# Performance work log

Measured on AMD Instinct MI355X. Metric: run time of the kernel, lower is better.

Reference implementation:

```python
import jax, jax.numpy as jnp
import numpy as np

MAX_NORM = 10.0
NUM_LAYERS = 3
MARGIN = 0.1
VAE_BETA = 0.1
EPS = 1e-7
N_NODES = 100000


def logmap0(x):
    # Lorentz (k=1) log map at origin: first coord -> 0, spatial scaled
    x0 = x[..., :1]
    alpha = jnp.maximum(x0, 1.0 + EPS)
    coef = jnp.arccosh(alpha) / jnp.sqrt(jnp.maximum(alpha * alpha - 1.0, EPS))
    return jnp.concatenate([jnp.zeros_like(x0), coef * x[..., 1:]], axis=-1)


def expmap0(u, project=False):
    # Lorentz (k=1) exp map at origin; first coord of u is ignored (tangent at o)
    sp = u[..., 1:]
    n = jnp.maximum(jnp.linalg.norm(sp, axis=-1, keepdims=True), EPS)
    x_sp = jnp.sinh(n) / n * sp
    if project:
        sn = jnp.linalg.norm(x_sp, axis=-1, keepdims=True)
        x_sp = x_sp * jnp.minimum(1.0, MAX_NORM / jnp.maximum(sn, EPS))
        x0 = jnp.sqrt(1.0 + jnp.sum(x_sp * x_sp, axis=-1, keepdims=True))
    else:
        x0 = jnp.cosh(n)
    return jnp.concatenate([x0, x_sp], axis=-1)


def sqdist(x, y):
    inner = -x[..., 0] * y[..., 0] + jnp.sum(x[..., 1:] * y[..., 1:], axis=-1)
    d = jnp.arccosh(jnp.maximum(-inner, 1.0 + EPS))
    return d * d


def moe(x, W, b, gW, gb):
    gates = jax.nn.softmax(x @ gW + gb, axis=-1)              # [N,E]
    expert = jnp.einsum('nd,edo->neo', x, W) + b               # [N,E,D]
    return jnp.einsum('neo,ne->no', expert, gates)             # [N,D]


def spmm(rows, cols, vals, h):
    return jax.ops.segment_sum(vals[:, None] * h[cols], rows, num_segments=N_NODES)


def setup_inputs() -> dict:
    key = jax.random.key(0)
    ks = jax.random.split(key, 24)
    D, E, NNZ, T = 64, 8, 3200000, 262144
    Nu, Ni = 60000, 40000
    s = 0.05
    emb_user = expmap0(jax.random.normal(ks[0], (Nu, D)) * 0.1, project=True)
    emb_item = expmap0(jax.random.normal(ks[1], (Ni, D)) * 0.1, project=True)
    return {
        'emb_user': emb_user,
        'emb_item': emb_item,
        'adj_rows': jax.random.randint(ks[2], (NNZ,), 0, N_NODES, dtype=jnp.int32),
        'adj_cols': jax.random.randint(ks[3], (NNZ,), 0, N_NODES, dtype=jnp.int32),
        'adj_vals': jax.random.uniform(ks[4], (NNZ,)) * 0.05,
        'triples': jax.random.randint(ks[5], (T, 3), 0, N_NODES, dtype=jnp.int32),
        'eps': jax.random.normal(ks[6], (N_NODES, D)),
        'tW': jax.random.normal(ks[7], (E, D, D)) * s,
        'tb': jax.random.normal(ks[8], (E, D)) * s,
        'tgW': jax.random.normal(ks[9], (D, E)) * s,
        'tgb': jax.random.normal(ks[10], (E,)) * s,
        'muW': jax.random.normal(ks[11], (D, D)) * s,
        'mub': jax.random.normal(ks[12], (D,)) * s,
        'lvW': jax.random.normal(ks[13], (D, D)) * s,
        'lvb': jax.random.normal(ks[14], (D,)) * s,
        'f1W': jax.random.normal(ks[15], (D, 2 * D)) * s,
        'f1b': jax.random.normal(ks[16], (2 * D,)) * s,
        'f2W': jax.random.normal(ks[17], (2 * D, D)) * s,
        'f2b': jax.random.normal(ks[18], (D,)) * s,
        'dW': jax.random.normal(ks[19], (E, D, D)) * s,
        'db': jax.random.normal(ks[20], (E, D)) * s,
        'dgW': jax.random.normal(ks[21], (D, E)) * s,
        'dgb': jax.random.normal(ks[22], (E,)) * s,
    }


def reference(emb_user, emb_item, adj_rows, adj_cols, adj_vals, triples, eps,
              tW, tb, tgW, tgb, muW, mub, lvW, lvb,
              f1W, f1b, f2W, f2b, dW, db, dgW, dgb):
    # encode: log map frozen hyperbolic embeddings, MoE transform
    t = jnp.concatenate([logmap0(emb_user), logmap0(emb_item)], axis=0)   # [N,D]
    m = moe(t, tW, tb, tgW, tgb)                                          # [N,D]
    # VAE
    mu = m @ muW + mub
    logvar = m @ lvW + lvb
    std = jnp.exp(0.5 * logvar)
    z = expmap0(mu + eps * std, project=True)
    # hyperbolic decoder
    h = logmap0(z)
    h = jax.nn.relu(h @ f1W + f1b)
    h = h @ f2W + f2b
    h = moe(h, dW, db, dgW, dgb)
    recon = expmap0(h, project=True)
    recon_loss = jnp.mean(sqdist(recon, expmap0(m)))
    kl_loss = -0.5 * jnp.mean(1.0 + logvar - mu * mu - jnp.exp(logvar))
    # margin loss: num_layers of sparse propagation, sum of layer outputs
    res = m
    out_sum = jnp.zeros_like(m)
    for _ in range(NUM_LAYERS):
        res = spmm(adj_rows, adj_cols, adj_vals, res)
        out_sum = out_sum + res
    out = expmap0(out_sum, project=True)
    a, p, n = out[triples[:, 0]], out[triples[:, 1]], out[triples[:, 2]]
    margin_loss = jnp.sum(jax.nn.relu(sqdist(a, p) - sqdist(a, n) + MARGIN))
    return margin_loss + VAE_BETA * (recon_loss + kl_loss)
```

## Files before the change

### kernel.cpp

```cpp
#include <hip/hip_runtime.h>
#include <math.h>

#define EPSF 1e-7f
#define MAXNRM 10.0f
#define NB 782
#define RPB 128
#define EPT 16

using bf16x8 = __attribute__((ext_vector_type(8))) short;
using f32x4  = __attribute__((ext_vector_type(4))) float;

__device__ __forceinline__ float wsum(float v) {
    #pragma unroll
    for (int off = 32; off > 0; off >>= 1) v += __shfl_xor(v, off, 64);
    return v;
}

__device__ __forceinline__ unsigned short f2bf(float x) {
    unsigned u = __float_as_uint(x);
    unsigned r = (u + 0x7FFFu + ((u >> 16) & 1u)) >> 16;
    return (unsigned short)r;
}
__device__ __forceinline__ float bflo(unsigned u) { return __uint_as_float(u << 16); }
__device__ __forceinline__ float bfhi(unsigned u) { return __uint_as_float(u & 0xFFFF0000u); }

__global__ __launch_bounds__(256) void k_logmap(const float* __restrict__ eu, const float* __restrict__ ei,
                                                int Nu, int Ntot, float* __restrict__ out) {
    const int lane = threadIdx.x & 63;
    const int g = lane >> 4, q = lane & 15;
    const int n = blockIdx.x * 16 + (threadIdx.x >> 6) * 4 + g;
    if (n >= Ntot) return;
    const float* src = (n < Nu) ? (eu + (size_t)n * 64) : (ei + (size_t)(n - Nu) * 64);
    const float x0 = src[0];
    const float alpha = fmaxf(x0, 1.0f + EPSF);
    const float coef = acoshf(alpha) / sqrtf(fmaxf(alpha * alpha - 1.0f, EPSF));
    const float4 v = *(const float4*)(src + q * 4);
    float4 o;
    o.x = (q == 0) ? 0.0f : coef * v.x;
    o.y = coef * v.y; o.z = coef * v.z; o.w = coef * v.w;
    *(float4*)(out + ((size_t)n << 6) + q * 4) = o;
}

__global__ __launch_bounds__(256) void k_prep(const float* __restrict__ W, const float* __restrict__ Bb,
                                              unsigned short* __restrict__ Wt, unsigned short* __restrict__ Bt) {
    const int i = blockIdx.x * 256 + threadIdx.x;
    if (i < 4096) {
        const int e = i >> 9, o = (i >> 3) & 63, db = i & 7;
        unsigned short v[8];
        #pragma unroll
        for (int j = 0; j < 8; ++j)
            v[j] = f2bf(W[((size_t)e << 12) + (size_t)(db * 8 + j) * 64 + o]);
        uint4 p;
        p.x = (unsigned)v[0] | ((unsigned)v[1] << 16);
        p.y = (unsigned)v[2] | ((unsigned)v[3] << 16);
        p.z = (unsigned)v[4] | ((unsigned)v[5] << 16);
        p.w = (unsigned)v[6] | ((unsigned)v[7] << 16);
        *(uint4*)(Wt + (((size_t)(e * 64 + o)) << 6) + db * 8) = p;
    } else if (i < 4096 + 512) {
        const int j = i - 4096, o = j >> 3, e = j & 7;
        Bt[o * 8 + e] = f2bf(Bb[e * 64 + o]);
    }
}

__global__ __launch_bounds__(256) void k_prepw(const float* __restrict__ src,
                                               unsigned short* __restrict__ dst, int K, int O) {
    const int i = blockIdx.x * 256 + threadIdx.x;
    if (i >= K * O) return;
    const int o = i / K, k = i - o * K;
    dst[i] = f2bf(src[k * O + o]);
}

__global__ __launch_bounds__(256) void k_moe_mfma(
    const float* __restrict__ X, float* __restrict__ Y,
    const unsigned short* __restrict__ Wt, const unsigned short* __restrict__ Bt,
    const float* __restrict__ GW, const float* __restrict__ GB,
    unsigned short* __restrict__ Bhout, int Ntot)
{
    __shared__ float sX[64][68];
    __shared__ float sG[64][8];
    __shared__ float sGW[512];
    const int tid = threadIdx.x;
    const int n0 = blockIdx.x * 64;

    for (int i = tid; i < 64 * 16; i += 256) {
        const int rr = i >> 4, cc = i & 15;
        float4 v = make_float4(0.f, 0.f, 0.f, 0.f);
        if (n0 + rr < Ntot) v = *(const float4*)(X + (size_t)(n0 + rr) * 64 + cc * 4);
        *(float4*)&sX[rr][cc * 4] = v;
    }
    for (int i = tid; i < 512; i += 256) sGW[i] = GW[i];
    __syncthreads();

    {
        const int n = tid >> 2, e0 = (tid & 3) * 2;
        float lg0 = GB[e0], lg1 = GB[e0 + 1];
        #pragma unroll 8
        for (int d = 0; d < 64; ++d) {
            const float xv = sX[n][d];
            lg0 += xv * sGW[d * 8 + e0];
            lg1 += xv * sGW[d * 8 + e0 + 1];
        }
        sG[n][e0] = lg0; sG[n][e0 + 1] = lg1;
    }
    __syncthreads();
    if (tid < 64) {
        float ex[8], mx = -1e30f, s = 0.f;
        #pragma unroll
        for (int e = 0; e < 8; ++e) mx = fmaxf(mx, sG[tid][e]);
        #pragma unroll
        for (int e = 0; e < 8; ++e) { ex[e] = expf(sG[tid][e] - mx); s += ex[e]; }
        const float inv = 1.0f / s;
        #pragma unroll
        for (int e = 0; e < 8; ++e) sG[tid][e] = ex[e] * inv;
    }
    __syncthreads();

    const int w = tid >> 6, l = tid & 63;
    const int m = l & 15, kq = l >> 4;
    const int col = w * 16 + m;

    f32x4 zero = {0.f, 0.f, 0.f, 0.f};
    f32x4 acc[4];
    #pragma unroll
    for (int rt = 0; rt < 4; ++rt) acc[rt] = zero;

    bf16x8 bcur = *(const bf16x8*)(Wt + (((size_t)col) << 6) + kq * 8);

    #pragma unroll
    for (int kk = 0; kk < 16; ++kk) {
        const int e = kk >> 1;
        const int d0 = (kk & 1) * 32 + kq * 8;
        bf16x8 bnext = bcur;
        if (kk < 15) {
            const int e2 = (kk + 1) >> 1;
            const int d02 = ((kk + 1) & 1) * 32 + kq * 8;
            bnext = *(const bf16x8*)(Wt + (((size_t)(e2 * 64 + col)) << 6) + d02);
        }
        #pragma unroll
        for (int rt = 0; rt < 4; ++rt) {
            const int row = rt * 16 + m;
            const float gme = sG[row][e];
            const float4 xa = *(const float4*)&sX[row][d0];
            const float4 xb = *(const float4*)&sX[row][d0 + 4];
            union { bf16x8 v; unsigned short u[8]; } af;
            af.u[0] = f2bf(gme * xa.x); af.u[1] = f2bf(gme * xa.y);
            af.u[2] = f2bf(gme * xa.z); af.u[3] = f2bf(gme * xa.w);
            af.u[4] = f2bf(gme * xb.x); af.u[5] = f2bf(gme * xb.y);
            af.u[6] = f2bf(gme * xb.z); af.u[7] = f2bf(gme * xb.w);
            acc[rt] = __builtin_amdgcn_mfma_f32_16x16x32_bf16(af.v, bcur, acc[rt], 0, 0, 0);
        }
        bcur = bnext;
    }
    {
        bf16x8 z8 = {0, 0, 0, 0, 0, 0, 0, 0};
        bf16x8 bb = z8;
        if (kq == 0) bb = *(const bf16x8*)(Bt + (col << 3));
        #pragma unroll
        for (int rt = 0; rt < 4; ++rt) {
            union { bf16x8 v; unsigned short u[8]; } af;
            #pragma unroll
            for (int j = 0; j < 8; ++j)
                af.u[j] = (kq == 0) ? f2bf(sG[rt * 16 + m][j]) : (unsigned short)0;
            acc[rt] = __builtin_amdgcn_mfma_f32_16x16x32_bf16(af.v, bb, acc[rt], 0, 0, 0);
        }
    }

    #pragma unroll
    for (int rt = 0; rt < 4; ++rt) {
        #pragma unroll
        for (int r = 0; r < 4; ++r) {
            const int row = rt * 16 + kq * 4 + r;
            if (n0 + row < Ntot) {
                Y[(size_t)(n0 + row) * 64 + col] = acc[rt][r];
                if (Bhout)
                    Bhout[(((size_t)(n0 + row)) << 6) + col] = f2bf(acc[rt][r]);
            }
        }
    }
}

__global__ __launch_bounds__(256) void k_vae_mfma(
    const float* __restrict__ M, float* __restrict__ Hout,
    const float* __restrict__ EPSN, const unsigned short* __restrict__ WtV,
    const float* __restrict__ mub, const float* __restrict__ lvb,
    float* __restrict__ klslot, int Ntot)
{
    __shared__ float sX[64][68];
    __shared__ float sC[64];
    const int tid = threadIdx.x;
    const int n0 = blockIdx.x * 64;

    for (int i = tid; i < 64 * 16; i += 256) {
        const int rr = i >> 4, cc = i & 15;
        float4 v = make_float4(0.f, 0.f, 0.f, 0.f);
        if (n0 + rr < Ntot) v = *(const float4*)(M + (size_t)(n0 + rr) * 64 + cc * 4);
        *(float4*)&sX[rr][cc * 4] = v;
    }
    __syncthreads();

    const int w = tid >> 6, l = tid & 63;
    const int m = l & 15, kq = l >> 4;
    const int rowm = w * 16 + m;

    f32x4 zero = {0.f, 0.f, 0.f, 0.f};
    f32x4 acc[8];
    #pragma unroll
    for (int t = 0; t < 8; ++t) acc[t] = zero;

    #pragma unroll
    for (int ks = 0; ks < 2; ++ks) {
        const int k0 = ks * 32 + kq * 8;
        const float4 xa = *(const float4*)&sX[rowm][k0];
        const float4 xb = *(const float4*)&sX[rowm][k0 + 4];
        union { bf16x8 v; unsigned short u[8]; } af;
        af.u[0] = f2bf(xa.x); af.u[1] = f2bf(xa.y); af.u[2] = f2bf(xa.z); af.u[3] = f2bf(xa.w);
        af.u[4] = f2bf(xb.x); af.u[5] = f2bf(xb.y); af.u[6] = f2bf(xb.z); af.u[7] = f2bf(xb.w);
        #pragma unroll
        for (int t = 0; t < 8; ++t) {
            const bf16x8 bf = *(const bf16x8*)(WtV + (((size_t)(t * 16 + m)) << 6) + k0);
            acc[t] = __builtin_amdgcn_mfma_f32_16x16x32_bf16(af.v, bf, acc[t], 0, 0, 0);
        }
    }

    float klp = 0.f;
    float uv[4][4];
    #pragma unroll
    for (int t = 0; t < 4; ++t) {
        const int col = t * 16 + m;
        const float mb = mub[col], lb = lvb[col];
        #pragma unroll
        for (int r = 0; r < 4; ++r) {
            const int row = w * 16 + kq * 4 + r;
            const float mu = acc[t][r] + mb;
            const float lv = acc[t + 4][r] + lb;
            const float elv = expf(lv);
            float ep = 0.f;
            if (n0 + row < Ntot) {
                klp += 1.0f + lv - mu * mu - elv;
                ep = EPSN[(size_t)(n0 + row) * 64 + col];
            }
            uv[t][r] = mu + ep * expf(0.5f * lv);
        }
    }
    klp = wsum(klp);
    if (l == 0) atomicAdd(&klslot[(blockIdx.x * 4 + w) & 255], klp);

    #pragma unroll
    for (int t = 0; t < 4; ++t)
        #pragma unroll
        for (int r = 0; r < 4; ++r)
            sX[w * 16 + kq * 4 + r][t * 16 + m] = uv[t][r];
    __syncthreads();

    {
        const int r2 = tid >> 2, j = tid & 3;
        float ss = 0.f;
        #pragma unroll
        for (int jj = 0; jj < 4; ++jj) {
            float4 a = *(const float4*)&sX[r2][j * 16 + jj * 4];
            if (j == 0 && jj == 0) a.x = 0.f;
            ss += a.x * a.x + a.y * a.y + a.z * a.z + a.w * a.w;
        }
        ss += __shfl_xor(ss, 1, 64);
        ss += __shfl_xor(ss, 2, 64);
        if (j == 0) {
            const float nr = fmaxf(sqrtf(ss), EPSF);
            const float r = sinhf(nr) / nr;
            const float sn = r * sqrtf(ss);
            const float scale = fminf(1.0f, MAXNRM / fmaxf(sn, EPSF));
            const float mult = r * scale;
            const float s2 = mult * mult * ss;
            const float z0 = sqrtf(1.0f + s2);
            const float alpha = fmaxf(z0, 1.0f + EPSF);
            const float coef = acoshf(alpha) / sqrtf(fmaxf(alpha * alpha - 1.0f, EPSF));
            sC[r2] = coef * mult;
        }
    }
    __syncthreads();

    for (int i = tid; i < 64 * 16; i += 256) {
        const int rr = i >> 4, cc = i & 15;
        if (n0 + rr >= Ntot) continue;
        const float4 v = *(const float4*)&sX[rr][cc * 4];
        const float sc = sC[rr];
        float4 o;
        o.x = (cc == 0) ? 0.f : sc * v.x;
        o.y = sc * v.y; o.z = sc * v.z; o.w = sc * v.w;
        *(float4*)(Hout + (size_t)(n0 + rr) * 64 + cc * 4) = o;
    }
}

__global__ __launch_bounds__(256) void k_ffn_mfma(
    float* __restrict__ Hio,
    const unsigned short* __restrict__ Wt1f, const float* __restrict__ f1b,
    const unsigned short* __restrict__ Wt2f, const float* __restrict__ f2b, int Ntot)
{
    __shared__ float sH[64][68];
    __shared__ unsigned short sH1[64][136];
    const int tid = threadIdx.x;
    const int n0 = blockIdx.x * 64;

    for (int i = tid; i < 64 * 16; i += 256) {
        const int rr = i >> 4, cc = i & 15;
        float4 v = make_float4(0.f, 0.f, 0.f, 0.f);
        if (n0 + rr < Ntot) v = *(const float4*)(Hio + (size_t)(n0 + rr) * 64 + cc * 4);
        *(float4*)&sH[rr][cc * 4] = v;
    }
    __syncthreads();

    const int w = tid >> 6, l = tid & 63;
    const int m = l & 15, kq = l >> 4;
    const int rowm = w * 16 + m;

    f32x4 zero = {0.f, 0.f, 0.f, 0.f};
    f32x4 acc1[8];
    #pragma unroll
    for (int t = 0; t < 8; ++t) acc1[t] = zero;

    #pragma unroll
    for (int ks = 0; ks < 2; ++ks) {
        const int k0 = ks * 32 + kq * 8;
        const float4 xa = *(const float4*)&sH[rowm][k0];
        const float4 xb = *(const float4*)&sH[rowm][k0 + 4];
        union { bf16x8 v; unsigned short u[8]; } af;
        af.u[0] = f2bf(xa.x); af.u[1] = f2bf(xa.y); af.u[2] = f2bf(xa.z); af.u[3] = f2bf(xa.w);
        af.u[4] = f2bf(xb.x); af.u[5] = f2bf(xb.y); af.u[6] = f2bf(xb.z); af.u[7] = f2bf(xb.w);
        #pragma unroll
        for (int t = 0; t < 8; ++t) {
            const bf16x8 bf = *(const bf16x8*)(Wt1f + (((size_t)(t * 16 + m)) << 6) + k0);
            acc1[t] = __builtin_amdgcn_mfma_f32_16x16x32_bf16(af.v, bf, acc1[t], 0, 0, 0);
        }
    }
    #pragma unroll
    for (int t = 0; t < 8; ++t) {
        const float bb = f1b[t * 16 + m];
        #pragma unroll
        for (int r = 0; r < 4; ++r)
            sH1[w * 16 + kq * 4 + r][t * 16 + m] = f2bf(fmaxf(acc1[t][r] + bb, 0.f));
    }
    __syncthreads();

    f32x4 acc2[4];
    #pragma unroll
    for (int t = 0; t < 4; ++t) acc2[t] = zero;
    #pragma unroll
    for (int ks = 0; ks < 4; ++ks) {
        const int k0 = ks * 32 + kq * 8;
        const bf16x8 af = *(const bf16x8*)&sH1[rowm][k0];
        #pragma unroll
        for (int t = 0; t < 4; ++t) {
            const bf16x8 bf = *(const bf16x8*)(Wt2f + (((size_t)(t * 16 + m)) << 7) + k0);
            acc2[t] = __builtin_amdgcn_mfma_f32_16x16x32_bf16(af, bf, acc2[t], 0, 0, 0);
        }
    }
    #pragma unroll
    for (int t = 0; t < 4; ++t) {
        const float bb = f2b[t * 16 + m];
        #pragma unroll
        for (int r = 0; r < 4; ++r) {
            const int row = w * 16 + kq * 4 + r;
            if (n0 + row < Ntot)
                Hio[(size_t)(n0 + row) * 64 + t * 16 + m] = acc2[t][r] + bb;
        }
    }
}

__global__ __launch_bounds__(256) void k_recon(
    const float* __restrict__ HM, const float* __restrict__ M,
    int Ntot, float* __restrict__ slot)
{
    const int lane = threadIdx.x & 63;
    const int g = lane >> 4, q = lane & 15;
    const int n = blockIdx.x * 16 + (threadIdx.x >> 6) * 4 + g;

    float ssh = 0.f, ssm = 0.f, dot = 0.f;
    if (n < Ntot) {
        const float4 h = *(const float4*)(HM + ((size_t)n << 6) + q * 4);
        const float4 m = *(const float4*)(M  + ((size_t)n << 6) + q * 4);
        const float hx = (q == 0) ? 0.f : h.x;
        const float mx = (q == 0) ? 0.f : m.x;
        ssh = hx * hx + h.y * h.y + h.z * h.z + h.w * h.w;
        ssm = mx * mx + m.y * m.y + m.z * m.z + m.w * m.w;
        dot = hx * mx + h.y * m.y + h.z * m.z + h.w * m.w;
    }
    #pragma unroll
    for (int off = 1; off < 16; off <<= 1) {
        ssh += __shfl_xor(ssh, off, 64);
        ssm += __shfl_xor(ssm, off, 64);
        dot += __shfl_xor(dot, off, 64);
    }

    float part = 0.f;
    if (q == 0 && n < Ntot) {
        const float nm = fmaxf(sqrtf(ssm), EPSF);
        const float em0 = coshf(nm);
        const float rm = sinhf(nm) / nm;

        const float nh = fmaxf(sqrtf(ssh), EPSF);
        const float rh = sinhf(nh) / nh;
        const float sn = rh * sqrtf(ssh);
        const float scale = fminf(1.0f, MAXNRM / fmaxf(sn, EPSF));
        const float mult = rh * scale;
        const float rec0 = sqrtf(1.0f + mult * mult * ssh);

        const float inner = mult * rm * dot - rec0 * em0;
        const float dd = acoshf(fmaxf(-inner, 1.0f + EPSF));
        part = dd * dd;
    }
    part = wsum(part);
    __shared__ float sb[4];
    if (lane == 0) sb[threadIdx.x >> 6] = part;
    __syncthreads();
    if (threadIdx.x == 0)
        atomicAdd(&slot[blockIdx.x & 255], sb[0] + sb[1] + sb[2] + sb[3]);
}

__global__ __launch_bounds__(256) void k_bhist(const int* __restrict__ rows, int nnz,
                                               int* __restrict__ bhist) {
    __shared__ int h[NB];
    for (int j = threadIdx.x; j < NB; j += 256) h[j] = 0;
    __syncthreads();
    for (int i = blockIdx.x * 256 + threadIdx.x; i < nnz; i += gridDim.x * 256)
        atomicAdd(&h[rows[i] >> 7], 1);
    __syncthreads();
    for (int j = threadIdx.x; j < NB; j += 256)
        if (h[j]) atomicAdd(&bhist[j], h[j]);
}

__global__ __launch_bounds__(1024) void k_bscan(const int* __restrict__ bhist,
                                                int* __restrict__ bstart, int* __restrict__ gcur) {
    __shared__ int s[1024];
    const int tid = threadIdx.x;
    int v = (tid < NB) ? bhist[tid] : 0;
    s[tid] = v;
    __syncthreads();
    for (int off = 1; off < 1024; off <<= 1) {
        int t = (tid >= off) ? s[tid - off] : 0;
        __syncthreads();
        s[tid] += t;
        __syncthreads();
    }
    if (tid < NB) {
        bstart[tid + 1] = s[tid];
        gcur[tid] = s[tid] - v;
        if (tid == 0) bstart[0] = 0;
    }
}

__global__ __launch_bounds__(256) void k_bscatter(
    const int* __restrict__ rows, const int* __restrict__ cols,
    const float* __restrict__ vals, int nnz,
    int* __restrict__ gcur, int2* __restrict__ tmp)
{
    __shared__ int lh[NB];
    __shared__ int lb[NB];
    const int tid = threadIdx.x;
    for (int j = tid; j < NB; j += 256) lh[j] = 0;
    __syncthreads();

    const int base = blockIdx.x * (256 * EPT);
    int r[EPT], c[EPT], lp[EPT];
    float v[EPT];
    #pragma unroll
    for (int j = 0; j < EPT; ++j) {
        const int i = base + j * 256 + tid;
        if (i < nnz) {
            r[j] = rows[i]; c[j] = cols[i]; v[j] = vals[i];
            lp[j] = atomicAdd(&lh[r[j] >> 7], 1);
        }
    }
    __syncthreads();
    for (int j = tid; j < NB; j += 256)
        if (lh[j]) lb[j] = atomicAdd(&gcur[j], lh[j]);
    __syncthreads();
    #pragma unroll
    for (int j = 0; j < EPT; ++j) {
        const int i = base + j * 256 + tid;
        if (i < nnz) {
            int2 e;
            e.x = ((r[j] & 127) << 17) | c[j];
            e.y = __float_as_int(v[j]);
            tmp[lb[r[j] >> 7] + lp[j]] = e;
        }
    }
}

__global__ __launch_bounds__(256) void k_sort(
    const int2* __restrict__ tmp, const int* __restrict__ bstart,
    int2* __restrict__ sedge, int* __restrict__ Fout, int Ntot, int nnz)
{
    __shared__ int cnt[RPB];
    __shared__ int excl[RPB];
    const int b = blockIdx.x;
    const int tid = threadIdx.x;
    if (tid < RPB) cnt[tid] = 0;
    __syncthreads();
    const int s = bstart[b], t = bstart[b + 1];

    for (int i = s + tid; i < t; i += 256)
        atomicAdd(&cnt[((unsigned)tmp[i].x) >> 17], 1);
    __syncthreads();

    if (tid < 64) {
        const int a0 = cnt[2 * tid], a1 = cnt[2 * tid + 1];
        const int pairsum = a0 + a1;
        int run = pairsum;
        #pragma unroll
        for (int off = 1; off < 64; off <<= 1) {
            const int vv = __shfl_up(run, off, 64);
            if (tid >= off) run += vv;
        }
        const int ep = run - pairsum;
        excl[2 * tid] = ep;
        excl[2 * tid + 1] = ep + a0;
    }
    __syncthreads();

    const int r0 = b << 7;
    if (tid < RPB) {
        const int r = r0 + tid;
        if (r < Ntot) Fout[r] = s + excl[tid];
        cnt[tid] = excl[tid];
    }
    if (b == NB - 1 && tid == 0) Fout[Ntot] = nnz;
    __syncthreads();

    for (int i = s + tid; i < t; i += 256) {
        const int2 e = tmp[i];
        const int rib = ((unsigned)e.x) >> 17;
        const int lpos = atomicAdd(&cnt[rib], 1);
        int2 o; o.x = e.x & 0x1FFFF; o.y = e.y;
        sedge[s + lpos] = o;
    }
}

__global__ __launch_bounds__(256) void k_spmm(
    const unsigned short* __restrict__ in, unsigned short* __restrict__ outb,
    const int* __restrict__ F, const int2* __restrict__ sedge, int Ntot, int nnz)
{
    const int r = blockIdx.x * 4 + (threadIdx.x >> 6);
    if (r >= Ntot) return;
    const int lane = threadIdx.x & 63;
    const int g = lane >> 3, q = lane & 7;
    const int e0 = F[r], e1 = F[r + 1];
    const int nnzm1 = nnz - 1;

    float acc0[8], acc1[8];
    #pragma unroll
    for (int j = 0; j < 8; ++j) { acc0[j] = 0.f; acc1[j] = 0.f; }

    int2 edA, edB;
    uint4 hbA, hbB;
    {
        const int ea = e0 + g, eb = e0 + 8 + g;
        edA = sedge[min(ea, nnzm1)]; if (ea >= e1) edA.y = 0;
        edB = sedge[min(eb, nnzm1)]; if (eb >= e1) edB.y = 0;
        hbA = *(const uint4*)(in + (((size_t)edA.x) << 6) + q * 8);
        hbB = *(const uint4*)(in + (((size_t)edB.x) << 6) + q * 8);
    }

    for (int base = e0; base < e1; base += 16) {
        const int na = base + 16 + g, nb = base + 24 + g;
        int2 edA2 = sedge[min(na, nnzm1)]; if (na >= e1) edA2.y = 0;
        int2 edB2 = sedge[min(nb, nnzm1)]; if (nb >= e1) edB2.y = 0;
        const uint4 hbA2 = *(const uint4*)(in + (((size_t)edA2.x) << 6) + q * 8);
        const uint4 hbB2 = *(const uint4*)(in + (((size_t)edB2.x) << 6) + q * 8);

        {
            const float v = __int_as_float(edA.y);
            acc0[0] += v * bflo(hbA.x);
            acc0[1] += v * bfhi(hbA.x);
            acc0[2] += v * bflo(hbA.y);
            acc0[3] += v * bfhi(hbA.y);
            acc0[4] += v * bflo(hbA.z);
            acc0[5] += v * bfhi(hbA.z);
            acc0[6] += v * bflo(hbA.w);
            acc0[7] += v * bfhi(hbA.w);
        }
        {
            const float v = __int_as_float(edB.y);
            acc1[0] += v * bflo(hbB.x);
            acc1[1] += v * bfhi(hbB.x);
            acc1[2] += v * bflo(hbB.y);
            acc1[3] += v * bfhi(hbB.y);
            acc1[4] += v * bflo(hbB.z);
            acc1[5] += v * bfhi(hbB.z);
            acc1[6] += v * bflo(hbB.w);
            acc1[7] += v * bfhi(hbB.w);
        }
        edA = edA2; edB = edB2; hbA = hbA2; hbB = hbB2;
    }
    float a0[8];
    #pragma unroll
    for (int j = 0; j < 8; ++j) a0[j] = acc0[j] + acc1[j];

    #pragma unroll
    for (int off = 8; off < 64; off <<= 1)
        #pragma unroll
        for (int j = 0; j < 8; ++j) a0[j] += __shfl_xor(a0[j], off, 64);

    if (g == 0) {
        const size_t ob = (((size_t)r) << 6) + q * 8;
        uint4 p;
        p.x = (unsigned)f2bf(a0[0]) | ((unsigned)f2bf(a0[1]) << 16);
        p.y = (unsigned)f2bf(a0[2]) | ((unsigned)f2bf(a0[3]) << 16);
        p.z = (unsigned)f2bf(a0[4]) | ((unsigned)f2bf(a0[5]) << 16);
        p.w = (unsigned)f2bf(a0[6]) | ((unsigned)f2bf(a0[7]) << 16);
        *(uint4*)(outb + ob) = p;
    }
}

__global__ __launch_bounds__(256) void k_osum(
    const unsigned short* __restrict__ r1, const unsigned short* __restrict__ r2,
    const unsigned short* __restrict__ r3, unsigned short* __restrict__ outb, int Ntot)
{
    const int lane = threadIdx.x & 63;
    const int g = lane >> 4, q = lane & 15;
    const int n = blockIdx.x * 16 + (threadIdx.x >> 6) * 4 + g;
    if (n >= Ntot) return;
    const size_t ob = ((size_t)n << 6) + q * 4;
    const uint2 a = *(const uint2*)(r1 + ob);
    const uint2 b = *(const uint2*)(r2 + ob);
    const uint2 c = *(const uint2*)(r3 + ob);
    float s0 = bflo(a.x) + bflo(b.x) + bflo(c.x);
    float s1 = bfhi(a.x) + bfhi(b.x) + bfhi(c.x);
    float s2 = bflo(a.y) + bflo(b.y) + bflo(c.y);
    float s3 = bfhi(a.y) + bfhi(b.y) + bfhi(c.y);
    const float v0 = (q == 0) ? 0.f : s0;
    float ss = v0 * v0 + s1 * s1 + s2 * s2 + s3 * s3;
    #pragma unroll
    for (int off = 1; off < 16; off <<= 1) ss += __shfl_xor(ss, off, 64);
    const float nr = fmaxf(sqrtf(ss), EPSF);
    const float r = sinhf(nr) / nr;
    const float sn = r * sqrtf(ss);
    const float scale = fminf(1.0f, MAXNRM / fmaxf(sn, EPSF));
    const float mult = r * scale;
    const float o0 = (q == 0) ? sqrtf(1.0f + mult * mult * ss) : mult * s0;
    uint2 p;
    p.x = (unsigned)f2bf(o0) | ((unsigned)f2bf(mult * s1) << 16);
    p.y = (unsigned)f2bf(mult * s2) | ((unsigned)f2bf(mult * s3) << 16);
    *(uint2*)(outb + ob) = p;
}

__global__ __launch_bounds__(256) void k_triples(
    const unsigned short* __restrict__ Ob, const int* __restrict__ tri,
    int T, float* __restrict__ slot)
{
    const int lane = threadIdx.x & 63;
    const int g = lane >> 4, q = lane & 15;
    const int wid = blockIdx.x * 4 + (threadIdx.x >> 6);
    const int stride = gridDim.x * 4 * 4;

    float racc = 0.f;
    int t = wid * 4 + g;

    uint2 ca, cp, cn;
    if (t < T) {
        const int a = tri[3 * t], p = tri[3 * t + 1], nn = tri[3 * t + 2];
        ca = *(const uint2*)(Ob + (((size_t)a) << 6) + q * 4);
        cp = *(const uint2*)(Ob + (((size_t)p) << 6) + q * 4);
        cn = *(const uint2*)(Ob + (((size_t)nn) << 6) + q * 4);
    }

    for (; t < T; ) {
        const int tn = t + stride;
        const int tc = min(tn, T - 1);
        const int a2 = tri[3 * tc], p2 = tri[3 * tc + 1], n2 = tri[3 * tc + 2];
        const uint2 na_ = *(const uint2*)(Ob + (((size_t)a2) << 6) + q * 4);
        const uint2 np_ = *(const uint2*)(Ob + (((size_t)p2) << 6) + q * 4);
        const uint2 nn_ = *(const uint2*)(Ob + (((size_t)n2) << 6) + q * 4);

        {
            const float a0 = bflo(ca.x), a1 = bfhi(ca.x), a2f = bflo(ca.y), a3 = bfhi(ca.y);
            const float p0 = bflo(cp.x), p1 = bfhi(cp.x), p2f = bflo(cp.y), p3 = bfhi(cp.y);
            const float n0 = bflo(cn.x), n1 = bfhi(cn.x), n2f = bflo(cn.y), n3 = bfhi(cn.y);
            const float s0 = (q == 0) ? -1.f : 1.f;
            float i1 = s0 * a0 * p0 + a1 * p1 + a2f * p2f + a3 * p3;
            float i2 = s0 * a0 * n0 + a1 * n1 + a2f * n2f + a3 * n3;
            #pragma unroll
            for (int off = 1; off < 16; off <<= 1) {
                i1 += __shfl_xor(i1, off, 64);
                i2 += __shfl_xor(i2, off, 64);
            }
            if (q == 0) {
                const float d1 = acoshf(fmaxf(-i1, 1.0f + EPSF));
                const float d2 = acoshf(fmaxf(-i2, 1.0f + EPSF));
                const float l = d1 * d1 - d2 * d2 + 0.1f;
                if (l > 0.f) racc += l;
            }
        }
        ca = na_; cp = np_; cn = nn_;
        t = tn;
    }

    racc = wsum(racc);
    __shared__ float sb[4];
    if (lane == 0) sb[threadIdx.x >> 6] = racc;
    __syncthreads();
// ... 14 lines not shown
        const float R = sr[0] + sr[1] + sr[2] + sr[3];
        const float K = sk[0] + sk[1] + sk[2] + sk[3];
        const float recon = R / (float)Ntot;
        const float kl = -0.5f * K / ((float)Ntot * 64.0f);
        out[0] = M + 0.1f * (recon + kl);
    }
}

extern "C" void kernel_launch(void* const* d_in, const int* in_sizes, int n_in,
                              void* d_out, int out_size, void* d_ws, size_t ws_size,
                              hipStream_t stream)
{
    const float* emb_user = (const float*)d_in[0];
    const float* emb_item = (const float*)d_in[1];
    const int*   adj_rows = (const int*)d_in[2];
    const int*   adj_cols = (const int*)d_in[3];
    const float* adj_vals = (const float*)d_in[4];
    const int*   triples  = (const int*)d_in[5];
    const float* epsin    = (const float*)d_in[6];
    const float* tW  = (const float*)d_in[7];
    const float* tb  = (const float*)d_in[8];
    const float* tgW = (const float*)d_in[9];
    const float* tgb = (const float*)d_in[10];
    const float* muW = (const float*)d_in[11];
    const float* mub = (const float*)d_in[12];
    const float* lvW = (const float*)d_in[13];
    const float* lvb = (const float*)d_in[14];
    const float* f1W = (const float*)d_in[15];
    const float* f1b = (const float*)d_in[16];
    const float* f2W = (const float*)d_in[17];
    const float* f2b = (const float*)d_in[18];
    const float* dW  = (const float*)d_in[19];
    const float* db  = (const float*)d_in[20];
    const float* dgW = (const float*)d_in[21];
    const float* dgb = (const float*)d_in[22];

    const int Nu = in_sizes[0] / 64, Ni = in_sizes[1] / 64;
    const int N = Nu + Ni;
    const int NNZ = in_sizes[4];
    const int T = in_sizes[5] / 3;

    float* ws = (float*)d_ws;
    size_t off = 0;
    float* slots = ws + off; off += 1024;
    float* A  = ws + off; off += (size_t)N * 64;
    float* B  = ws + off; off += (size_t)N * 64;
    float* C  = ws + off; off += (size_t)N * 64;
    float* D  = ws + off; off += (size_t)N * 64;
    float* E  = ws + off; off += (size_t)N * 64;
    int*   F  = (int*)(ws + off); off += (size_t)N + 64;
    int*   bstart = (int*)(ws + off); off += 1024;
    int*   bhist  = (int*)(ws + off); off += 1024;
    int*   gcur   = (int*)(ws + off); off += 1024;
    unsigned short* Wt1 = (unsigned short*)(ws + off); off += 16384;
    unsigned short* Bt1 = (unsigned short*)(ws + off); off += 256;
    unsigned short* Wt2 = (unsigned short*)(ws + off); off += 16384;
    unsigned short* Bt2 = (unsigned short*)(ws + off); off += 256;
    unsigned short* WtV  = (unsigned short*)(ws + off); off += 4096;
    unsigned short* Wt1f = (unsigned short*)(ws + off); off += 4096;
    unsigned short* Wt2f = (unsigned short*)(ws + off); off += 4096;

    int2* tmp   = (int2*)A;
    int2* sedge = (int2*)D;
    unsigned short* Bh  = (unsigned short*)E;
    unsigned short* Hb1 = (unsigned short*)E + (size_t)N * 64;
    unsigned short* Hb2 = (unsigned short*)C;
    unsigned short* Hb3 = (unsigned short*)A;
    unsigned short* Ob  = (unsigned short*)B;

    hipMemsetAsync(slots, 0, 1024 * sizeof(float), stream);
    hipMemsetAsync(bhist, 0, 1024 * sizeof(int), stream);

    const int nb16 = (N + 15) / 16;
    const int nb64 = (N + 63) / 64;

    k_prep<<<18, 256, 0, stream>>>(tW, tb, Wt1, Bt1);
    k_prep<<<18, 256, 0, stream>>>(dW, db, Wt2, Bt2);
    k_prepw<<<16, 256, 0, stream>>>(muW, WtV, 64, 64);
    k_prepw<<<16, 256, 0, stream>>>(lvW, WtV + 4096, 64, 64);
    k_prepw<<<32, 256, 0, stream>>>(f1W, Wt1f, 64, 128);
    k_prepw<<<32, 256, 0, stream>>>(f2W, Wt2f, 128, 64);

    k_logmap<<<nb16, 256, 0, stream>>>(emb_user, emb_item, Nu, N, A);
    k_moe_mfma<<<nb64, 256, 0, stream>>>(A, B, Wt1, Bt1, tgW, tgb, Bh, N);
    k_vae_mfma<<<nb64, 256, 0, stream>>>(B, A, epsin, WtV, mub, lvb, slots + 512, N);
    k_ffn_mfma<<<nb64, 256, 0, stream>>>(A, Wt1f, f1b, Wt2f, f2b, N);
    k_moe_mfma<<<nb64, 256, 0, stream>>>(A, C, Wt2, Bt2, dgW, dgb, nullptr, N);
    k_recon<<<nb16, 256, 0, stream>>>(C, B, N, slots + 256);

    k_bhist<<<512, 256, 0, stream>>>(adj_rows, NNZ, bhist);
    k_bscan<<<1, 1024, 0, stream>>>(bhist, bstart, gcur);
    const int ns1 = (NNZ + 256 * EPT - 1) / (256 * EPT);
    k_bscatter<<<ns1, 256, 0, stream>>>(adj_rows, adj_cols, adj_vals, NNZ, gcur, tmp);
    k_sort<<<NB, 256, 0, stream>>>(tmp, bstart, sedge, F, N, NNZ);

    k_spmm<<<(N + 3) / 4, 256, 0, stream>>>(Bh,  Hb1, F, sedge, N, NNZ);
    k_spmm<<<(N + 3) / 4, 256, 0, stream>>>(Hb1, Hb2, F, sedge, N, NNZ);
    k_spmm<<<(N + 3) / 4, 256, 0, stream>>>(Hb2, Hb3, F, sedge, N, NNZ);

    k_osum<<<nb16, 256, 0, stream>>>(Hb1, Hb2, Hb3, Ob, N);

    k_triples<<<2048, 256, 0, stream>>>(Ob, triples, T, slots);
    k_final<<<1, 256, 0, stream>>>(slots, (float*)d_out, N);
}
```

Measured before the change: 513.2 us.

## Fuse independent dense and sparse-sort kernels into combined launches

Merges the six weight-prep kernels into one launch. It also pairs independent stages into 'fat' kernels that dispatch on block index: logmap with the row histogram, encoder MoE with the bucket scatter, and VAE with the per-bucket sort. The goal is to cut launch count and let the memory-bound CSR build overlap with the MFMA-heavy dense stages. The tmp buffer moves from A to C so it does not collide with buffers live in the merged stages. The merged kernels share one shared-memory size, which may lower occupancy for the lighter branches.

```diff
diff --git a/kernel.cpp b/kernel.cpp
--- a/kernel.cpp
+++ b/kernel.cpp
@@ -9,6 +9,7 @@
 
 using bf16x8 = __attribute__((ext_vector_type(8))) short;
 using f32x4  = __attribute__((ext_vector_type(4))) float;
+typedef unsigned short u16;
 
 __device__ __forceinline__ float wsum(float v) {
     #pragma unroll
@@ -16,19 +17,21 @@
     return v;
 }
 
-__device__ __forceinline__ unsigned short f2bf(float x) {
+__device__ __forceinline__ u16 f2bf(float x) {
     unsigned u = __float_as_uint(x);
     unsigned r = (u + 0x7FFFu + ((u >> 16) & 1u)) >> 16;
-    return (unsigned short)r;
+    return (u16)r;
 }
 __device__ __forceinline__ float bflo(unsigned u) { return __uint_as_float(u << 16); }
 __device__ __forceinline__ float bfhi(unsigned u) { return __uint_as_float(u & 0xFFFF0000u); }
 
-__global__ __launch_bounds__(256) void k_logmap(const float* __restrict__ eu, const float* __restrict__ ei,
-                                                int Nu, int Ntot, float* __restrict__ out) {
+
+__device__ __forceinline__ void body_logmap(int bid, const float* __restrict__ eu,
+                                            const float* __restrict__ ei, int Nu, int Ntot,
+                                            float* __restrict__ out) {
     const int lane = threadIdx.x & 63;
     const int g = lane >> 4, q = lane & 15;
-    const int n = blockIdx.x * 16 + (threadIdx.x >> 6) * 4 + g;
+    const int n = bid * 16 + (threadIdx.x >> 6) * 4 + g;
     if (n >= Ntot) return;
     const float* src = (n < Nu) ? (eu + (size_t)n * 64) : (ei + (size_t)(n - Nu) * 64);
     const float x0 = src[0];
@@ -41,46 +44,28 @@
     *(float4*)(out + ((size_t)n << 6) + q * 4) = o;
 }
 
-__global__ __launch_bounds__(256) void k_prep(const float* __restrict__ W, const float* __restrict__ Bb,
-                                              unsigned short* __restrict__ Wt, unsigned short* __restrict__ Bt) {
-    const int i = blockIdx.x * 256 + threadIdx.x;
-    if (i < 4096) {
-        const int e = i >> 9, o = (i >> 3) & 63, db = i & 7;
-        unsigned short v[8];
-        #pragma unroll
-        for (int j = 0; j < 8; ++j)
-            v[j] = f2bf(W[((size_t)e << 12) + (size_t)(db * 8 + j) * 64 + o]);
-        uint4 p;
-        p.x = (unsigned)v[0] | ((unsigned)v[1] << 16);
-        p.y = (unsigned)v[2] | ((unsigned)v[3] << 16);
-        p.z = (unsigned)v[4] | ((unsigned)v[5] << 16);
-        p.w = (unsigned)v[6] | ((unsigned)v[7] << 16);
-        *(uint4*)(Wt + (((size_t)(e * 64 + o)) << 6) + db * 8) = p;
-    } else if (i < 4096 + 512) {
-        const int j = i - 4096, o = j >> 3, e = j & 7;
-        Bt[o * 8 + e] = f2bf(Bb[e * 64 + o]);
-    }
-}
-
-__global__ __launch_bounds__(256) void k_prepw(const float* __restrict__ src,
-                                               unsigned short* __restrict__ dst, int K, int O) {
-    const int i = blockIdx.x * 256 + threadIdx.x;
-    if (i >= K * O) return;
-    const int o = i / K, k = i - o * K;
-    dst[i] = f2bf(src[k * O + o]);
-}
-
-__global__ __launch_bounds__(256) void k_moe_mfma(
+__device__ __forceinline__ void body_bhist(int bid, int nblk, const int* __restrict__ rows,
+                                           int nnz, int* __restrict__ bhist, int* h) {
+    for (int j = threadIdx.x; j < NB; j += 256) h[j] = 0;
+    __syncthreads();
+    for (int i = bid * 256 + threadIdx.x; i < nnz; i += nblk * 256)
+        atomicAdd(&h[rows[i] >> 7], 1);
+    __syncthreads();
+    for (int j = threadIdx.x; j < NB; j += 256)
+        if (h[j]) atomicAdd(&bhist[j], h[j]);
+}
+
+__device__ __forceinline__ void body_moe(int bid, char* smem,
     const float* __restrict__ X, float* __restrict__ Y,
-    const unsigned short* __restrict__ Wt, const unsigned short* __restrict__ Bt,
+    const u16* __restrict__ Wt, const u16* __restrict__ Bt,
     const float* __restrict__ GW, const float* __restrict__ GB,
-    unsigned short* __restrict__ Bhout, int Ntot)
-{
-    __shared__ float sX[64][68];
-    __shared__ float sG[64][8];
-    __shared__ float sGW[512];
+    u16* __restrict__ Bhout, int Ntot)
+{
+    float (*sX)[68] = (float(*)[68])smem;
+    float (*sG)[8]  = (float(*)[8])(smem + 17408);
+    float* sGW      = (float*)(smem + 17408 + 2048);
     const int tid = threadIdx.x;
-    const int n0 = blockIdx.x * 64;
+    const int n0 = bid * 64;
 
     for (int i = tid; i < 64 * 16; i += 256) {
         const int rr = i >> 4, cc = i & 15;
@@ -142,7 +127,7 @@
             const float gme = sG[row][e];
             const float4 xa = *(const float4*)&sX[row][d0];
             const float4 xb = *(const float4*)&sX[row][d0 + 4];
-            union { bf16x8 v; unsigned short u[8]; } af;
+            union { bf16x8 v; u16 u[8]; } af;
             af.u[0] = f2bf(gme * xa.x); af.u[1] = f2bf(gme * xa.y);
             af.u[2] = f2bf(gme * xa.z); af.u[3] = f2bf(gme * xa.w);
             af.u[4] = f2bf(gme * xb.x); af.u[5] = f2bf(gme * xb.y);
@@ -157,10 +142,10 @@
         if (kq == 0) bb = *(const bf16x8*)(Bt + (col << 3));
         #pragma unroll
         for (int rt = 0; rt < 4; ++rt) {
-            union { bf16x8 v; unsigned short u[8]; } af;
+            union { bf16x8 v; u16 u[8]; } af;
             #pragma unroll
             for (int j = 0; j < 8; ++j)
-                af.u[j] = (kq == 0) ? f2bf(sG[rt * 16 + m][j]) : (unsigned short)0;
+                af.u[j] = (kq == 0) ? f2bf(sG[rt * 16 + m][j]) : (u16)0;
             acc[rt] = __builtin_amdgcn_mfma_f32_16x16x32_bf16(af.v, bb, acc[rt], 0, 0, 0);
         }
     }
@@ -179,16 +164,54 @@
     }
 }
 
-__global__ __launch_bounds__(256) void k_vae_mfma(
+__device__ __forceinline__ void body_bscatter(int bid, char* smem,
+    const int* __restrict__ rows, const int* __restrict__ cols,
+    const float* __restrict__ vals, int nnz,
+    int* __restrict__ gcur, int2* __restrict__ tmp)
+{
+    int* lh = (int*)smem;
+    int* lb = (int*)(smem + 3128);
+    const int tid = threadIdx.x;
+    for (int j = tid; j < NB; j += 256) lh[j] = 0;
+    __syncthreads();
+
+    const int base = bid * (256 * EPT);
+    int r[EPT], c[EPT], lp[EPT];
+    float v[EPT];
+    #pragma unroll
+    for (int j = 0; j < EPT; ++j) {
+        const int i = base + j * 256 + tid;
+        if (i < nnz) {
+            r[j] = rows[i]; c[j] = cols[i]; v[j] = vals[i];
+            lp[j] = atomicAdd(&lh[r[j] >> 7], 1);
+        }
+    }
+    __syncthreads();
+    for (int j = tid; j < NB; j += 256)
+        if (lh[j]) lb[j] = atomicAdd(&gcur[j], lh[j]);
+    __syncthreads();
+    #pragma unroll
+    for (int j = 0; j < EPT; ++j) {
+        const int i = base + j * 256 + tid;
+        if (i < nnz) {
+            int2 e;
+            e.x = ((r[j] & 127) << 17) | c[j];
+            e.y = __float_as_int(v[j]);
+            tmp[lb[r[j] >> 7] + lp[j]] = e;
+        }
+    }
+}
+
+__device__ __forceinline__ void body_vae(int bid, char* smem,
     const float* __restrict__ M, float* __restrict__ Hout,
-    const float* __restrict__ EPSN, const unsigned short* __restrict__ WtV,
+    const float* __restrict__ EPSN, const u16* __restrict__ WtV,
     const float* __restrict__ mub, const float* __restrict__ lvb,
     float* __restrict__ klslot, int Ntot)
 {
-    __shared__ float sX[64][68];
-    __shared__ float sC[64];
+    float (*sX)[68] = (float(*)[68])smem;
+    float* sC       = (float*)(smem + 17408);
     const int tid = threadIdx.x;
-    const int n0 = blockIdx.x * 64;
+    const int n0 = bid * 64;
 
     for (int i = tid; i < 64 * 16; i += 256) {
         const int rr = i >> 4, cc = i & 15;
@@ -212,7 +235,7 @@
         const int k0 = ks * 32 + kq * 8;
         const float4 xa = *(const float4*)&sX[rowm][k0];
         const float4 xb = *(const float4*)&sX[rowm][k0 + 4];
-        union { bf16x8 v; unsigned short u[8]; } af;
+        union { bf16x8 v; u16 u[8]; } af;
         af.u[0] = f2bf(xa.x); af.u[1] = f2bf(xa.y); af.u[2] = f2bf(xa.z); af.u[3] = f2bf(xa.w);
         af.u[4] = f2bf(xb.x); af.u[5] = f2bf(xb.y); af.u[6] = f2bf(xb.z); af.u[7] = f2bf(xb.w);
         #pragma unroll
@@ -243,7 +266,7 @@
         }
     }
     klp = wsum(klp);
-    if (l == 0) atomicAdd(&klslot[(blockIdx.x * 4 + w) & 255], klp);
+    if (l == 0) atomicAdd(&klslot[(bid * 4 + w) & 255], klp);
 
     #pragma unroll
     for (int t = 0; t < 4; ++t)
@@ -290,13 +313,192 @@
     }
 }
 
+__device__ __forceinline__ void body_sort(int bid, char* smem,
+    const int2* __restrict__ tmp, const int* __restrict__ bstart,
+    int2* __restrict__ sedge, int* __restrict__ Fout, int Ntot, int nnz)
+{
+    int* cnt  = (int*)smem;
+    int* excl = (int*)(smem + 512);
+    const int b = bid;
+    const int tid = threadIdx.x;
+    if (tid < RPB) cnt[tid] = 0;
+    __syncthreads();
+    const int s = bstart[b], t = bstart[b + 1];
+
+    for (int i = s + tid; i < t; i += 256)
+        atomicAdd(&cnt[((unsigned)tmp[i].x) >> 17], 1);
+    __syncthreads();
+
+    if (tid < 64) {
+        const int a0 = cnt[2 * tid], a1 = cnt[2 * tid + 1];
+        const int pairsum = a0 + a1;
+        int run = pairsum;
+        #pragma unroll
+        for (int off = 1; off < 64; off <<= 1) {
+            const int vv = __shfl_up(run, off, 64);
+            if (tid >= off) run += vv;
+        }
+        const int ep = run - pairsum;
+        excl[2 * tid] = ep;
+        excl[2 * tid + 1] = ep + a0;
+    }
+    __syncthreads();
+
+    const int r0 = b << 7;
+    if (tid < RPB) {
+        const int r = r0 + tid;
+        if (r < Ntot) Fout[r] = s + excl[tid];
+        cnt[tid] = excl[tid];
+    }
+    if (b == NB - 1 && tid == 0) Fout[Ntot] = nnz;
+    __syncthreads();
+
+    for (int i = s + tid; i < t; i += 256) {
+        const int2 e = tmp[i];
+        const int rib = ((unsigned)e.x) >> 17;
+        const int lpos = atomicAdd(&cnt[rib], 1);
+        int2 o; o.x = e.x & 0x1FFFF; o.y = e.y;
+        sedge[s + lpos] = o;
+    }
+}
+
+
+__global__ __launch_bounds__(256) void fat_prep(
+    const float* tW, const float* tb, u16* Wt1, u16* Bt1,
+    const float* dW, const float* db, u16* Wt2, u16* Bt2,
+    const float* muW, const float* lvW, u16* WtV,
+    const float* f1W, u16* Wt1f, const float* f2W, u16* Wt2f)
+{
+    const int b = blockIdx.x;
+    if (b < 36) {
+        const float* W = (b < 18) ? tW : dW;
+        const float* Bb = (b < 18) ? tb : db;
+        u16* Wt = (b < 18) ? Wt1 : Wt2;
+        u16* Bt = (b < 18) ? Bt1 : Bt2;
+        const int i = (b % 18) * 256 + threadIdx.x;
+        if (i < 4096) {
+            const int e = i >> 9, o = (i >> 3) & 63, dbi = i & 7;
+            u16 v[8];
+            #pragma unroll
+            for (int j = 0; j < 8; ++j)
+                v[j] = f2bf(W[((size_t)e << 12) + (size_t)(dbi * 8 + j) * 64 + o]);
+            uint4 p;
+            p.x = (unsigned)v[0] | ((unsigned)v[1] << 16);
+            p.y = (unsigned)v[2] | ((unsigned)v[3] << 16);
+            p.z = (unsigned)v[4] | ((unsigned)v[5] << 16);
+            p.w = (unsigned)v[6] | ((unsigned)v[7] << 16);
+            *(uint4*)(Wt + (((size_t)(e * 64 + o)) << 6) + dbi * 8) = p;
+        } else if (i < 4096 + 512) {
+            const int j = i - 4096, o = j >> 3, e = j & 7;
+            Bt[o * 8 + e] = f2bf(Bb[e * 64 + o]);
+        }
+    } else if (b < 68) {
+        const bool is_mu = (b < 52);
+        const float* src = is_mu ? muW : lvW;
+        u16* dst = is_mu ? WtV : (WtV + 4096);
+        const int i = ((b - (is_mu ? 36 : 52))) * 256 + threadIdx.x;
+        if (i < 4096) {
+            const int o = i / 64, k = i - o * 64;
+            dst[i] = f2bf(src[k * 64 + o]);
+        }
+    } else if (b < 100) {
+        const int i = (b - 68) * 256 + threadIdx.x;
+        if (i < 8192) {
+            const int o = i / 64, k = i - o * 64;
+            Wt1f[i] = f2bf(f1W[k * 128 + o]);
+        }
+    } else {
+        const int i = (b - 100) * 256 + threadIdx.x;
+        if (i < 8192) {
+            const int o = i / 128, k = i - o * 128;
+            Wt2f[i] = f2bf(f2W[k * 64 + o]);
+        }
+    }
+}
+
+#define NB_LOG 6250
+#define NB_HIST 512
+__global__ __launch_bounds__(256) void fat_log_bhist(
+    const float* eu, const float* ei, int Nu, int Ntot, float* out,
+    const int* rows, int nnz, int* bhist)
+{
+    __shared__ int h[NB];
+    const int b = blockIdx.x;
+    if (b < NB_LOG) {
+        body_logmap(b, eu, ei, Nu, Ntot, out);
+    } else {
+        body_bhist(b - NB_LOG, NB_HIST, rows, nnz, bhist, h);
+    }
+}
+
+#define NB_MOE 1563
+__global__ __launch_bounds__(256) void fat_moe_bsc(
+    const float* X, float* Y, const u16* Wt, const u16* Bt,
+    const float* GW, const float* GB, u16* Bhout, int Ntot,
+    const int* rows, const int* cols, const float* vals, int nnz,
+    int* gcur, int2* tmp)
+{
+    __shared__ __align__(16) char smem[21504];
+    const int b = blockIdx.x;
+    if (b < NB_MOE) {
+        body_moe(b, smem, X, Y, Wt, Bt, GW, GB, Bhout, Ntot);
+    } else {
+        body_bscatter(b - NB_MOE, smem, rows, cols, vals, nnz, gcur, tmp);
+    }
+}
+
+__global__ __launch_bounds__(256) void fat_vae_sort(
+    const float* M, float* Hout, const float* EPSN, const u16* WtV,
+    const float* mub, const float* lvb, float* klslot, int Ntot,
+    const int2* tmp, const int* bstart, int2* sedge, int* Fout, int nnz)
+{
+    __shared__ __align__(16) char smem[17664];
+    const int b = blockIdx.x;
+    if (b < NB_MOE) {
+        body_vae(b, smem, M, Hout, EPSN, WtV, mub, lvb, klslot, Ntot);
+    } else {
+        body_sort(b - NB_MOE, smem, tmp, bstart, sedge, Fout, Ntot, nnz);
+    }
+}
+
+
+__global__ __launch_bounds__(256) void k_moe_mfma(
+    const float* __restrict__ X, float* __restrict__ Y,
+    const u16* __restrict__ Wt, const u16* __restrict__ Bt,
+    const float* __restrict__ GW, const float* __restrict__ GB,
+    u16* __restrict__ Bhout, int Ntot)
+{
+    __shared__ __align__(16) char smem[21504];
+    body_moe(blockIdx.x, smem, X, Y, Wt, Bt, GW, GB, Bhout, Ntot);
+}
+
+__global__ __launch_bounds__(1024) void k_bscan(const int* __restrict__ bhist,
+                                                int* __restrict__ bstart, int* __restrict__ gcur) {
+    __shared__ int s[1024];
+    const int tid = threadIdx.x;
+    int v = (tid < NB) ? bhist[tid] : 0;
+    s[tid] = v;
+    __syncthreads();
+    for (int off = 1; off < 1024; off <<= 1) {
+        int t = (tid >= off) ? s[tid - off] : 0;
+        __syncthreads();
+        s[tid] += t;
+        __syncthreads();
+    }
+    if (tid < NB) {
+        bstart[tid + 1] = s[tid];
+        gcur[tid] = s[tid] - v;
+        if (tid == 0) bstart[0] = 0;
+    }
+}
+
 __global__ __launch_bounds__(256) void k_ffn_mfma(
     float* __restrict__ Hio,
-    const unsigned short* __restrict__ Wt1f, const float* __restrict__ f1b,
-    const unsigned short* __restrict__ Wt2f, const float* __restrict__ f2b, int Ntot)
+    const u16* __restrict__ Wt1f, const float* __restrict__ f1b,
+    const u16* __restrict__ Wt2f, const float* __restrict__ f2b, int Ntot)
 {
     __shared__ float sH[64][68];
-    __shared__ unsigned short sH1[64][136];
+    __shared__ u16 sH1[64][136];
     const int tid = threadIdx.x;
     const int n0 = blockIdx.x * 64;
 
@@ -322,7 +524,7 @@
         const int k0 = ks * 32 + kq * 8;
         const float4 xa = *(const float4*)&sH[rowm][k0];
         const float4 xb = *(const float4*)&sH[rowm][k0 + 4];
-        union { bf16x8 v; unsigned short u[8]; } af;
+        union { bf16x8 v; u16 u[8]; } af;
         af.u[0] = f2bf(xa.x); af.u[1] = f2bf(xa.y); af.u[2] = f2bf(xa.z); af.u[3] = f2bf(xa.w);
         af.u[4] = f2bf(xb.x); af.u[5] = f2bf(xb.y); af.u[6] = f2bf(xb.z); af.u[7] = f2bf(xb.w);
         #pragma unroll
@@ -415,127 +617,8 @@
         atomicAdd(&slot[blockIdx.x & 255], sb[0] + sb[1] + sb[2] + sb[3]);
 }
 
-__global__ __launch_bounds__(256) void k_bhist(const int* __restrict__ rows, int nnz,
-                                               int* __restrict__ bhist) {
-    __shared__ int h[NB];
-    for (int j = threadIdx.x; j < NB; j += 256) h[j] = 0;
-    __syncthreads();
-    for (int i = blockIdx.x * 256 + threadIdx.x; i < nnz; i += gridDim.x * 256)
-        atomicAdd(&h[rows[i] >> 7], 1);
-    __syncthreads();
-    for (int j = threadIdx.x; j < NB; j += 256)
-        if (h[j]) atomicAdd(&bhist[j], h[j]);
-}
-
-__global__ __launch_bounds__(1024) void k_bscan(const int* __restrict__ bhist,
-                                                int* __restrict__ bstart, int* __restrict__ gcur) {
-    __shared__ int s[1024];
-    const int tid = threadIdx.x;
-    int v = (tid < NB) ? bhist[tid] : 0;
-    s[tid] = v;
-    __syncthreads();
-    for (int off = 1; off < 1024; off <<= 1) {
-        int t = (tid >= off) ? s[tid - off] : 0;
-        __syncthreads();
-        s[tid] += t;
-        __syncthreads();
-    }
-    if (tid < NB) {
-        bstart[tid + 1] = s[tid];
-        gcur[tid] = s[tid] - v;
-        if (tid == 0) bstart[0] = 0;
-    }
-}
-
-__global__ __launch_bounds__(256) void k_bscatter(
-    const int* __restrict__ rows, const int* __restrict__ cols,
-    const float* __restrict__ vals, int nnz,
-    int* __restrict__ gcur, int2* __restrict__ tmp)
-{
-    __shared__ int lh[NB];
-    __shared__ int lb[NB];
-    const int tid = threadIdx.x;
-    for (int j = tid; j < NB; j += 256) lh[j] = 0;
-    __syncthreads();
-
-    const int base = blockIdx.x * (256 * EPT);
-    int r[EPT], c[EPT], lp[EPT];
-    float v[EPT];
-    #pragma unroll
-    for (int j = 0; j < EPT; ++j) {
-        const int i = base + j * 256 + tid;
-        if (i < nnz) {
-            r[j] = rows[i]; c[j] = cols[i]; v[j] = vals[i];
-            lp[j] = atomicAdd(&lh[r[j] >> 7], 1);
-        }
-    }
-    __syncthreads();
-    for (int j = tid; j < NB; j += 256)
-        if (lh[j]) lb[j] = atomicAdd(&gcur[j], lh[j]);
-    __syncthreads();
-    #pragma unroll
-    for (int j = 0; j < EPT; ++j) {
-        const int i = base + j * 256 + tid;
-        if (i < nnz) {
-            int2 e;
-            e.x = ((r[j] & 127) << 17) | c[j];
-            e.y = __float_as_int(v[j]);
-            tmp[lb[r[j] >> 7] + lp[j]] = e;
-        }
-    }
-}
-
-__global__ __launch_bounds__(256) void k_sort(
-    const int2* __restrict__ tmp, const int* __restrict__ bstart,
-    int2* __restrict__ sedge, int* __restrict__ Fout, int Ntot, int nnz)
-{
-    __shared__ int cnt[RPB];
-    __shared__ int excl[RPB];
-    const int b = blockIdx.x;
-    const int tid = threadIdx.x;
-    if (tid < RPB) cnt[tid] = 0;
-    __syncthreads();
-    const int s = bstart[b], t = bstart[b + 1];
-
-    for (int i = s + tid; i < t; i += 256)
-        atomicAdd(&cnt[((unsigned)tmp[i].x) >> 17], 1);
-    __syncthreads();
-
-    if (tid < 64) {
-        const int a0 = cnt[2 * tid], a1 = cnt[2 * tid + 1];
-        const int pairsum = a0 + a1;
-        int run = pairsum;
-        #pragma unroll
-        for (int off = 1; off < 64; off <<= 1) {
-            const int vv = __shfl_up(run, off, 64);
-            if (tid >= off) run += vv;
-        }
-        const int ep = run - pairsum;
-        excl[2 * tid] = ep;
-        excl[2 * tid + 1] = ep + a0;
-    }
-    __syncthreads();
-
-    const int r0 = b << 7;
-    if (tid < RPB) {
-        const int r = r0 + tid;
-        if (r < Ntot) Fout[r] = s + excl[tid];
-        cnt[tid] = excl[tid];
-    }
-    if (b == NB - 1 && tid == 0) Fout[Ntot] = nnz;
-    __syncthreads();
-
-    for (int i = s + tid; i < t; i += 256) {
-        const int2 e = tmp[i];
-        const int rib = ((unsigned)e.x) >> 17;
-        const int lpos = atomicAdd(&cnt[rib], 1);
-        int2 o; o.x = e.x & 0x1FFFF; o.y = e.y;
-        sedge[s + lpos] = o;
-    }
-}
-
 __global__ __launch_bounds__(256) void k_spmm(
-    const unsigned short* __restrict__ in, unsigned short* __restrict__ outb,
+    const u16* __restrict__ in, u16* __restrict__ outb,
     const int* __restrict__ F, const int2* __restrict__ sedge, int Ntot, int nnz)
 {
     const int r = blockIdx.x * 4 + (threadIdx.x >> 6);
@@ -611,8 +694,8 @@
 }
 
 __global__ __launch_bounds__(256) void k_osum(
-    const unsigned short* __restrict__ r1, const unsigned short* __restrict__ r2,
-    const unsigned short* __restrict__ r3, unsigned short* __restrict__ outb, int Ntot)
+    const u16* __restrict__ r1, const u16* __restrict__ r2,
+    const u16* __restrict__ r3, u16* __restrict__ outb, int Ntot)
 {
     const int lane = threadIdx.x & 63;
     const int g = lane >> 4, q = lane & 15;
@@ -643,7 +726,7 @@
 }
 
 __global__ __launch_bounds__(256) void k_triples(
-    const unsigned short* __restrict__ Ob, const int* __restrict__ tri,
+    const u16* __restrict__ Ob, const int* __restrict__ tri,
     int T, float* __restrict__ slot)
 {
     const int lane = threadIdx.x & 63;
@@ -764,48 +847,47 @@
     int*   bstart = (int*)(ws + off); off += 1024;
     int*   bhist  = (int*)(ws + off); off += 1024;
     int*   gcur   = (int*)(ws + off); off += 1024;
-    unsigned short* Wt1 = (unsigned short*)(ws + off); off += 16384;
-    unsigned short* Bt1 = (unsigned short*)(ws + off); off += 256;
-    unsigned short* Wt2 = (unsigned short*)(ws + off); off += 16384;
-    unsigned short* Bt2 = (unsigned short*)(ws + off); off += 256;
-    unsigned short* WtV  = (unsigned short*)(ws + off); off += 4096;
-    unsigned short* Wt1f = (unsigned short*)(ws + off); off += 4096;
-    unsigned short* Wt2f = (unsigned short*)(ws + off); off += 4096;
-
-    int2* tmp   = (int2*)A;
+    u16* Wt1 = (u16*)(ws + off); off += 16384;
+    u16* Bt1 = (u16*)(ws + off); off += 256;
+    u16* Wt2 = (u16*)(ws + off); off += 16384;
+    u16* Bt2 = (u16*)(ws + off); off += 256;
+    u16* WtV  = (u16*)(ws + off); off += 4096;
+    u16* Wt1f = (u16*)(ws + off); off += 4096;
+    u16* Wt2f = (u16*)(ws + off); off += 4096;
+
+    int2* tmp   = (int2*)C;
     int2* sedge = (int2*)D;
-    unsigned short* Bh  = (unsigned short*)E;
-    unsigned short* Hb1 = (unsigned short*)E + (size_t)N * 64;
-    unsigned short* Hb2 = (unsigned short*)C;
-    unsigned short* Hb3 = (unsigned short*)A;
-    unsigned short* Ob  = (unsigned short*)B;
+    u16* Bh  = (u16*)E;
+    u16* Hb1 = (u16*)E + (size_t)N * 64;
+    u16* Hb2 = (u16*)C;
+    u16* Hb3 = (u16*)A;
+    u16* Ob  = (u16*)B;
 
     hipMemsetAsync(slots, 0, 1024 * sizeof(float), stream);
     hipMemsetAsync(bhist, 0, 1024 * sizeof(int), stream);
 
     const int nb16 = (N + 15) / 16;
     const int nb64 = (N + 63) / 64;
-
-    k_prep<<<18, 256, 0, stream>>>(tW, tb, Wt1, Bt1);
-    k_prep<<<18, 256, 0, stream>>>(dW, db, Wt2, Bt2);
-    k_prepw<<<16, 256, 0, stream>>>(muW, WtV, 64, 64);
-    k_prepw<<<16, 256, 0, stream>>>(lvW, WtV + 4096, 64, 64);
-    k_prepw<<<32, 256, 0, stream>>>(f1W, Wt1f, 64, 128);
-    k_prepw<<<32, 256, 0, stream>>>(f2W, Wt2f, 128, 64);
-
-    k_logmap<<<nb16, 256, 0, stream>>>(emb_user, emb_item, Nu, N, A);
-    k_moe_mfma<<<nb64, 256, 0, stream>>>(A, B, Wt1, Bt1, tgW, tgb, Bh, N);
-    k_vae_mfma<<<nb64, 256, 0, stream>>>(B, A, epsin, WtV, mub, lvb, slots + 512, N);
+    const int ns1 = (NNZ + 256 * EPT - 1) / (256 * EPT);
+
+    fat_prep<<<132, 256, 0, stream>>>(tW, tb, Wt1, Bt1, dW, db, Wt2, Bt2,
+                                      muW, lvW, WtV, f1W, Wt1f, f2W, Wt2f);
+
+    fat_log_bhist<<<NB_LOG + NB_HIST, 256, 0, stream>>>(emb_user, emb_item, Nu, N, A,
+                                                        adj_rows, NNZ, bhist);
+
+    k_bscan<<<1, 1024, 0, stream>>>(bhist, bstart, gcur);
+
+    fat_moe_bsc<<<NB_MOE + 782, 256, 0, stream>>>(A, B, Wt1, Bt1, tgW, tgb, Bh, N,
+                                                  adj_rows, adj_cols, adj_vals, NNZ, gcur, tmp);
+
+    fat_vae_sort<<<NB_MOE + NB, 256, 0, stream>>>(B, A, epsin, WtV, mub, lvb, slots + 512, N,
+                                                  tmp, bstart, sedge, F, NNZ);
+
     k_ffn_mfma<<<nb64, 256, 0, stream>>>(A, Wt1f, f1b, Wt2f, f2b, N);
     k_moe_mfma<<<nb64, 256, 0, stream>>>(A, C, Wt2, Bt2, dgW, dgb, nullptr, N);
     k_recon<<<nb16, 256, 0, stream>>>(C, B, N, slots + 256);
 
-    k_bhist<<<512, 256, 0, stream>>>(adj_rows, NNZ, bhist);
-    k_bscan<<<1, 1024, 0, stream>>>(bhist, bstart, gcur);
-    const int ns1 = (NNZ + 256 * EPT - 1) / (256 * EPT);
-    k_bscatter<<<ns1, 256, 0, stream>>>(adj_rows, adj_cols, adj_vals, NNZ, gcur, tmp);
-    k_sort<<<NB, 256, 0, stream>>>(tmp, bstart, sedge, F, N, NNZ);
-
     k_spmm<<<(N + 3) / 4, 256, 0, stream>>>(Bh,  Hb1, F, sedge, N, NNZ);
     k_spmm<<<(N + 3) / 4, 256, 0, stream>>>(Hb1, Hb2, F, sedge, N, NNZ);
     k_spmm<<<(N + 3) / 4, 256, 0, stream>>>(Hb2, Hb3, F, sedge, N, NNZ);
```

Result: faster. 459.7 us (-10.4%).
